# Kernel optimization log

Measured on AMD Instinct MI355X. Metric: run time of the kernel, lower is better.

## Reference

```python
import jax, jax.numpy as jnp
import numpy as np

NUM_HEADS = 16
NUM_KV_HEADS = 4
HEAD_DIM = 64
HIDDEN = 1024
B, S = 2, 2048


def setup_inputs() -> dict:
    key = jax.random.key(0)
    ks = jax.random.split(key, 9)
    sc = 0.02
    return {
        "x": jax.random.normal(ks[0], (B, S, HIDDEN), dtype=jnp.float32),
        "Wq": jax.random.normal(ks[1], (HIDDEN, NUM_HEADS * HEAD_DIM), dtype=jnp.float32) * sc,
        "bq": jnp.zeros((NUM_HEADS * HEAD_DIM,), dtype=jnp.float32),
        "Wk": jax.random.normal(ks[2], (HIDDEN, NUM_KV_HEADS * HEAD_DIM), dtype=jnp.float32) * sc,
        "bk": jnp.zeros((NUM_KV_HEADS * HEAD_DIM,), dtype=jnp.float32),
        "Wv": jax.random.normal(ks[3], (HIDDEN, NUM_KV_HEADS * HEAD_DIM), dtype=jnp.float32) * sc,
        "bv": jnp.zeros((NUM_KV_HEADS * HEAD_DIM,), dtype=jnp.float32),
        "Wo": jax.random.normal(ks[4], (NUM_HEADS * HEAD_DIM, HIDDEN), dtype=jnp.float32) * sc,
        "bo": jnp.zeros((HIDDEN,), dtype=jnp.float32),
    }


def reference(x, Wq, bq, Wk, bk, Wv, bv, Wo, bo):
    bs, seq, _ = x.shape
    groups = NUM_HEADS // NUM_KV_HEADS
    # projections -> [B, H, S, D]
    q = (x @ Wq + bq).reshape(bs, seq, NUM_HEADS, HEAD_DIM).transpose(0, 2, 1, 3)
    k = (x @ Wk + bk).reshape(bs, seq, NUM_KV_HEADS, HEAD_DIM).transpose(0, 2, 1, 3)
    v = (x @ Wv + bv).reshape(bs, seq, NUM_KV_HEADS, HEAD_DIM).transpose(0, 2, 1, 3)
    # repeat_interleave KV heads to match query heads (GQA expansion)
    k = jnp.repeat(k, groups, axis=1)
    v = jnp.repeat(v, groups, axis=1)
    # NOTE: source applies NO 1/sqrt(d) scaling and no mask/ALiBi
    scores = jnp.einsum("bhqd,bhkd->bhqk", q, k)
    attn = jax.nn.softmax(scores.astype(jnp.float32), axis=-1).astype(q.dtype)
    out = jnp.einsum("bhqk,bhkd->bhqd", attn, v)
    out = out.transpose(0, 2, 1, 3).reshape(bs, seq, NUM_HEADS * HEAD_DIM)
    return out @ Wo + bo
```

## Files before the change

### kernel.cpp

```cpp
#include <hip/hip_runtime.h>

#define NHEADS 16
#define NKV    4
#define HDIM   64
#define HIDDEN 1024
#define BATCH  2
#define SEQ    2048
#define MROWS  (BATCH * SEQ)
#define LOG2E  1.44269504088896340736f

typedef __bf16 bf16_t;
typedef bf16_t bf16x8 __attribute__((ext_vector_type(8)));
typedef float  f32x4  __attribute__((ext_vector_type(4)));

__device__ __forceinline__ float bf2f(unsigned short u) {
    return __uint_as_float(((unsigned int)u) << 16);
}
__device__ __forceinline__ unsigned short f2bf(float f) {
    unsigned int u = __float_as_uint(f);
    u += 0x7FFFu + ((u >> 16) & 1u);
    return (unsigned short)(u >> 16);
}

__device__ __forceinline__ void gld16(const unsigned short* g, unsigned short* l)
{
    __builtin_amdgcn_global_load_lds(
        (const __attribute__((address_space(1))) void*)g,
        (__attribute__((address_space(3))) void*)l,
        16, 0, 0);
}

__device__ __forceinline__ int swz(int row, int ch) {
    return (row * 8 + (ch ^ (row & 7))) * 8;
}
__device__ __forceinline__ int swz16(int row, int ch) {
    return (row * 16 + (ch ^ (row & 7))) * 8;
}

__device__ __forceinline__ bool sniff_is_f32(const unsigned short* __restrict__ x)
{
    const int e = (x[threadIdx.x & 63] >> 7) & 0xFF;
    const unsigned long long ok = __ballot(e >= 110 && e <= 140);
    return __popcll(ok) < 56;
}

__device__ __forceinline__ void load8cvt(const void* base, size_t elem, bool isf32, unsigned short out[8])
{
    if (!isf32) {
        *(uint4*)out = *(const uint4*)((const unsigned short*)base + elem);
    } else {
        const float* p = (const float*)base + elem;
        float4 v0 = *(const float4*)p;
        float4 v1 = *(const float4*)(p + 4);
        out[0] = f2bf(v0.x); out[1] = f2bf(v0.y); out[2] = f2bf(v0.z); out[3] = f2bf(v0.w);
        out[4] = f2bf(v1.x); out[5] = f2bf(v1.y); out[6] = f2bf(v1.z); out[7] = f2bf(v1.w);
    }
}
__device__ __forceinline__ float bias_at(const void* b, int i, bool isf32)
{
    return isf32 ? ((const float*)b)[i] : bf2f(((const unsigned short*)b)[i]);
}

__global__ __launch_bounds__(256)
void prep_kernel(const void* __restrict__ x,
                 const void* __restrict__ Wq, const void* __restrict__ Wk,
                 const void* __restrict__ Wv, const void* __restrict__ Wo,
                 unsigned short* __restrict__ xb,
                 unsigned short* __restrict__ Wqkvt,
                 unsigned short* __restrict__ Wot)
{
    const bool isf32 = sniff_is_f32((const unsigned short*)x);
    const int t = threadIdx.x;
    int bid = blockIdx.x;

    if (bid < 2048) {
        if (!isf32) return;
        const size_t c = (size_t)bid * 256 + t;
        unsigned short v[8];
        load8cvt(x, c * 8, true, v);
        *(uint4*)(&xb[c * 8]) = *(uint4*)v;
        return;
    }
    bid -= 2048;
    const void* src; unsigned short* dst; int N, rowoff;
    if (bid < 256)      {             src = Wq; dst = Wqkvt; N = 1024; rowoff = 0;    }
    else if (bid < 320) { bid -= 256; src = Wk; dst = Wqkvt; N = 256;  rowoff = 1024; }
    else if (bid < 384) { bid -= 320; src = Wv; dst = Wqkvt; N = 256;  rowoff = 1280; }
    else                { bid -= 384; src = Wo; dst = Wot;   N = 1024; rowoff = 0;    }
    const int ntx = N / 64;
    const int gn0 = (bid % ntx) * 64;
    const int gk0 = (bid / ntx) * 64;

    __shared__ unsigned short Ts[64][72];
#pragma unroll
    for (int half = 0; half < 2; ++half) {
        const int kl = (t >> 3) + half * 32;
        const int n8 = (t & 7) * 8;
        unsigned short v[8];
        load8cvt(src, (size_t)(gk0 + kl) * N + gn0 + n8, isf32, v);
        *(uint4*)(&Ts[kl][n8]) = *(uint4*)v;
    }
    __syncthreads();
#pragma unroll
    for (int half = 0; half < 2; ++half) {
        const int nl = (t >> 3) + half * 32;
        const int k8 = (t & 7) * 8;
        unsigned short v[8];
#pragma unroll
        for (int j = 0; j < 8; ++j) v[j] = Ts[k8 + j][nl];
        *(uint4*)(&dst[(size_t)(rowoff + gn0 + nl) * HIDDEN + gk0 + k8]) = *(uint4*)v;
    }
}

template<int TBM, int TBN>
__device__ __forceinline__ void gemm_tile(const unsigned short* __restrict__ A,
                                          const unsigned short* __restrict__ Bt,
                                          int K, int m0, int n0,
                                          unsigned short* As, unsigned short* Bs,
                                          f32x4 (&acc)[TBM / 32][TBN / 32])
{
    const int tid  = threadIdx.x;
    const int lane = tid & 63;
    const int wave = tid >> 6;
    const int quad = lane >> 4;
    const int l15  = lane & 15;
    const int wr   = wave >> 1;
    const int wc   = wave & 1;

    for (int k0 = 0; k0 < K; k0 += 128) {
#pragma unroll
        for (int r = 0; r < TBM / 16; ++r) {
            const int u = r * 256 + tid;
            const int row = u >> 4;
            const int gch = ((u & 15) ^ (row & 7)) * 8;
            gld16(&A[(size_t)(m0 + row) * K + k0 + gch], &As[(r * 256 + wave * 64) * 8]);
        }
#pragma unroll
        for (int r = 0; r < TBN / 16; ++r) {
            const int u = r * 256 + tid;
            const int row = u >> 4;
            const int gch = ((u & 15) ^ (row & 7)) * 8;
            gld16(&Bt[(size_t)(n0 + row) * K + k0 + gch], &Bs[(r * 256 + wave * 64) * 8]);
        }
        __syncthreads();

#pragma unroll
        for (int kk = 0; kk < 4; ++kk) {
            bf16x8 af[TBM / 32], bfv[TBN / 32];
#pragma unroll
            for (int i = 0; i < TBM / 32; ++i)
                af[i] = *(const bf16x8*)(&As[swz16(wr * (TBM / 2) + i * 16 + l15, kk * 4 + quad)]);
#pragma unroll
            for (int j = 0; j < TBN / 32; ++j)
                bfv[j] = *(const bf16x8*)(&Bs[swz16(wc * (TBN / 2) + j * 16 + l15, kk * 4 + quad)]);
#pragma unroll
            for (int i = 0; i < TBM / 32; ++i)
#pragma unroll
                for (int j = 0; j < TBN / 32; ++j)
                    acc[i][j] = __builtin_amdgcn_mfma_f32_16x16x32_bf16(af[i], bfv[j], acc[i][j], 0, 0, 0);
        }
        __syncthreads();
    }
}

__global__ __launch_bounds__(256)
void gemm_qkv(const void* __restrict__ xraw,
              const unsigned short* __restrict__ xb,
              const unsigned short* __restrict__ Bt,
              const void* __restrict__ bq, const void* __restrict__ bk,
              const void* __restrict__ bv,
              unsigned short* __restrict__ Qh,
              unsigned short* __restrict__ Kh,
              unsigned short* __restrict__ Vt)
{
    __shared__ __align__(16) unsigned short As[64 * 128];
    __shared__ __align__(16) unsigned short Bs[64 * 128];
    const bool bias_f32 = sniff_is_f32((const unsigned short*)xraw);
    const unsigned short* A = bias_f32 ? xb : (const unsigned short*)xraw;
    const int lane = threadIdx.x & 63;
    const int wave = threadIdx.x >> 6;
    const int quad = lane >> 4, l15 = lane & 15;
    const int wr = wave >> 1, wc = wave & 1;
    const int m0 = blockIdx.y * 64, n0 = blockIdx.x * 64;

    f32x4 acc[2][2] = {};
    gemm_tile<64, 64>(A, Bt, HIDDEN, m0, n0, As, Bs, acc);

#pragma unroll
    for (int i = 0; i < 2; ++i) {
#pragma unroll
        for (int j = 0; j < 2; ++j) {
            const int nn  = n0 + wc * 32 + j * 16 + l15;
            const int mmb = m0 + wr * 32 + i * 16 + quad * 4;
            const int b = mmb >> 11, s0 = mmb & 2047;
            if (nn < 1024) {
                const float bias = bias_at(bq, nn, bias_f32);
                const int h = nn >> 6, d = nn & 63;
                const size_t idx0 = (((size_t)(b * NHEADS + h)) * SEQ + s0) * 64 + d;
#pragma unroll
                for (int r = 0; r < 4; ++r)
                    Qh[idx0 + (size_t)r * 64] = f2bf((acc[i][j][r] + bias) * LOG2E);
            } else if (nn < 1280) {
                const int nk = nn - 1024;
                const float bias = bias_at(bk, nk, bias_f32);
                const int h = nk >> 6, d = nk & 63;
                const size_t idx0 = (((size_t)(b * NKV + h)) * SEQ + s0) * 64 + d;
#pragma unroll
                for (int r = 0; r < 4; ++r)
                    Kh[idx0 + (size_t)r * 64] = f2bf(acc[i][j][r] + bias);
            } else {
                const int nv = nn - 1280;
                const float bias = bias_at(bv, nv, bias_f32);
                const int h = nv >> 6, d = nv & 63;
                const size_t idx = (((size_t)(b * NKV + h)) * 64 + d) * SEQ + s0;
                unsigned short vv[4];
#pragma unroll
                for (int r = 0; r < 4; ++r) vv[r] = f2bf(acc[i][j][r] + bias);
                *(uint2*)(&Vt[idx]) = *(uint2*)vv;
            }
        }
    }
}

__global__ __launch_bounds__(256)
void gemm_o(const void* __restrict__ xraw,
            const unsigned short* __restrict__ A,
            const unsigned short* __restrict__ Bt,
            const void* __restrict__ bo,
            float* __restrict__ out)
{
    __shared__ __align__(16) unsigned short As[64 * 128];
    __shared__ __align__(16) unsigned short Bs[64 * 128];
    const bool bias_f32 = sniff_is_f32((const unsigned short*)xraw);
    const int lane = threadIdx.x & 63;
    const int wave = threadIdx.x >> 6;
    const int quad = lane >> 4, l15 = lane & 15;
    const int wr = wave >> 1, wc = wave & 1;
    const int m0 = blockIdx.y * 64, n0 = blockIdx.x * 64;

    f32x4 acc[2][2] = {};
    gemm_tile<64, 64>(A, Bt, HIDDEN, m0, n0, As, Bs, acc);

#pragma unroll
    for (int i = 0; i < 2; ++i) {
#pragma unroll
        for (int j = 0; j < 2; ++j) {
            const int nn = n0 + wc * 32 + j * 16 + l15;
            const float bvv = bias_at(bo, nn, bias_f32);
#pragma unroll
            for (int r = 0; r < 4; ++r) {
                const int mm = m0 + wr * 32 + i * 16 + quad * 4 + r;
                out[(size_t)mm * HIDDEN + nn] = acc[i][j][r] + bvv;
            }
        }
    }
}

#define PLD 68
__global__ __launch_bounds__(256)
void attn_kernel(const unsigned short* __restrict__ Qh,
                 const unsigned short* __restrict__ Kh,
                 const unsigned short* __restrict__ Vt,
                 unsigned short* __restrict__ O)
{
    __shared__ __align__(16) unsigned short Kth[64 * 64];
    __shared__ __align__(16) unsigned short VtT[64 * 64];
    __shared__ __align__(16) unsigned short Pt[4][16 * PLD];

    const int tid  = threadIdx.x;
    const int lane = tid & 63;
    const int wave = tid >> 6;
    const int quad = lane >> 4;
    const int l15  = lane & 15;

    const int qt = blockIdx.x;
    const int h  = blockIdx.y;
    const int b  = blockIdx.z;
    const int kv = h >> 2;

    const size_t qoff = ((size_t)(b * NHEADS + h)) * SEQ * HDIM;
    const size_t koff = ((size_t)(b * NKV + kv)) * SEQ * HDIM;
    const size_t voff = ((size_t)(b * NKV + kv)) * HDIM * SEQ;

    const int q0 = qt * 64 + wave * 16;

    const size_t qrow = qoff + (size_t)(q0 + l15) * HDIM;
    const bf16x8 qh0 = *(const bf16x8*)(&Qh[qrow + quad * 8]);
    const bf16x8 qh1 = *(const bf16x8*)(&Qh[qrow + 32 + quad * 8]);

    f32x4 o[4] = {};
    float lsum = 0.0f;

    const int srow0 = tid >> 3;
    const int schp  = tid & 7;

    const unsigned short* Khs = Kh + koff;
    const unsigned short* Vts = Vt + voff;

    for (int kt = 0; kt < SEQ / 64; ++kt, Khs += 64 * HDIM, Vts += 64) {
#pragma unroll
        for (int c = 0; c < 2; ++c) {
            const int row = srow0 + c * 32;
            const int gch = (schp ^ (row & 7)) * 8;
            gld16(&Khs[(size_t)row * 64 + gch],  &Kth[(c * 256 + wave * 64) * 8]);
            gld16(&Vts[(size_t)row * SEQ + gch], &VtT[(c * 256 + wave * 64) * 8]);
        }
        __syncthreads();

        f32x4 s[4];
#pragma unroll
        for (int j = 0; j < 4; ++j) {
            const int rr = j * 16 + l15;
            bf16x8 kh0 = *(const bf16x8*)(&Kth[swz(rr, quad)]);
            bf16x8 kh1 = *(const bf16x8*)(&Kth[swz(rr, quad ^ 4)]);
            f32x4 z = {};
            z = __builtin_amdgcn_mfma_f32_16x16x32_bf16(kh0, qh0, z, 0, 0, 0);
            s[j] = __builtin_amdgcn_mfma_f32_16x16x32_bf16(kh1, qh1, z, 0, 0, 0);
        }

#pragma unroll
        for (int j = 0; j < 4; ++j) {
            const float p0 = __builtin_amdgcn_exp2f(s[j][0]);
            const float p1 = __builtin_amdgcn_exp2f(s[j][1]);
            const float p2 = __builtin_amdgcn_exp2f(s[j][2]);
            const float p3 = __builtin_amdgcn_exp2f(s[j][3]);
            lsum += (p0 + p1) + (p2 + p3);
            uint2 w;
            w.x = __builtin_amdgcn_perm(__float_as_uint(p1), __float_as_uint(p0), 0x07060302u);
            w.y = __builtin_amdgcn_perm(__float_as_uint(p3), __float_as_uint(p2), 0x07060302u);
            *(uint2*)(&Pt[wave][l15 * PLD + j * 16 + quad * 4]) = w;
        }

#pragma unroll
        for (int kk = 0; kk < 2; ++kk) {
            bf16x8 pf = *(const bf16x8*)(&Pt[wave][l15 * PLD + kk * 32 + quad * 8]);
#pragma unroll
            for (int dt = 0; dt < 4; ++dt) {
                bf16x8 vf = *(const bf16x8*)(&VtT[swz(dt * 16 + l15, kk * 4 + quad)]);
                o[dt] = __builtin_amdgcn_mfma_f32_16x16x32_bf16(vf, pf, o[dt], 0, 0, 0);
            }
        }
        __syncthreads();
    }

    lsum += __shfl_xor(lsum, 16);
    lsum += __shfl_xor(lsum, 32);

    const float inv = 1.0f / lsum;
    const size_t rowbase = ((size_t)b * SEQ + (q0 + l15)) * (NHEADS * HDIM) + h * HDIM;
#pragma unroll
    for (int dt = 0; dt < 4; ++dt) {
        unsigned short v4[4];
#pragma unroll
        for (int r = 0; r < 4; ++r) v4[r] = f2bf(o[dt][r] * inv);
        *(uint2*)(&O[rowbase + dt * 16 + quad * 4]) = *(uint2*)v4;
    }
}

extern "C" void kernel_launch(void* const* d_in, const int* in_sizes, int n_in,
                              void* d_out, int out_size, void* d_ws, size_t ws_size,
                              hipStream_t stream)
{
    const void* x  = d_in[0];
    const void* Wq = d_in[1];
    const void* bq = d_in[2];
    const void* Wk = d_in[3];
    const void* bk = d_in[4];
    const void* Wv = d_in[5];
    const void* bv = d_in[6];
    const void* Wo = d_in[7];
    const void* bo = d_in[8];
    float* out = (float*)d_out;

    unsigned short* p = (unsigned short*)d_ws;
    unsigned short* xb    = p; p += (size_t)MROWS * HIDDEN;
    unsigned short* Wqkvt = p; p += (size_t)1536 * HIDDEN;
    unsigned short* Wot   = p; p += (size_t)HIDDEN * HIDDEN;
    unsigned short* Qh = p;  p += (size_t)MROWS * 1024;
    unsigned short* Kh = p;  p += (size_t)2 * NKV * SEQ * HDIM;
    unsigned short* Vt = p;  p += (size_t)2 * NKV * SEQ * HDIM;
    unsigned short* A2 = p;  p += (size_t)MROWS * 1024;

    dim3 blk(256);
    prep_kernel<<<dim3(2688), blk, 0, stream>>>(x, Wq, Wk, Wv, Wo, xb, Wqkvt, Wot);
    gemm_qkv<<<dim3(1536 / 64, MROWS / 64), blk, 0, stream>>>(
        x, xb, Wqkvt, bq, bk, bv, Qh, Kh, Vt);
    attn_kernel<<<dim3(SEQ / 64, NHEADS, BATCH), blk, 0, stream>>>(Qh, Kh, Vt, A2);
    gemm_o<<<dim3(1024 / 64, MROWS / 64), blk, 0, stream>>>(x, A2, Wot, bo, out);
}
```

Baseline: 186.5 us.

## Double-buffer attention K/V tiles, double query rows per wave, enlarge GEMM M tiles

The attention kernel now stages K/V tiles into two LDS buffers, prefetching the next tile while computing the current one, so there is one barrier per iteration instead of two. Each wave processes 32 query rows instead of 16, so each K/V fragment read is reused across two query sub-tiles and the attention grid halves. Both GEMMs move to 128x64 output tiles, giving more reuse of each B tile. The cost is more registers and LDS per block and fewer blocks in every kernel, which may lower occupancy.

```diff
diff --git a/kernel.cpp b/kernel.cpp
--- a/kernel.cpp
+++ b/kernel.cpp
@@ -173,7 +173,7 @@
               unsigned short* __restrict__ Kh,
               unsigned short* __restrict__ Vt)
 {
-    __shared__ __align__(16) unsigned short As[64 * 128];
+    __shared__ __align__(16) unsigned short As[128 * 128];
     __shared__ __align__(16) unsigned short Bs[64 * 128];
     const bool bias_f32 = sniff_is_f32((const unsigned short*)xraw);
     const unsigned short* A = bias_f32 ? xb : (const unsigned short*)xraw;
@@ -181,17 +181,17 @@
     const int wave = threadIdx.x >> 6;
     const int quad = lane >> 4, l15 = lane & 15;
     const int wr = wave >> 1, wc = wave & 1;
-    const int m0 = blockIdx.y * 64, n0 = blockIdx.x * 64;
-
-    f32x4 acc[2][2] = {};
-    gemm_tile<64, 64>(A, Bt, HIDDEN, m0, n0, As, Bs, acc);
-
-#pragma unroll
-    for (int i = 0; i < 2; ++i) {
+    const int m0 = blockIdx.y * 128, n0 = blockIdx.x * 64;
+
+    f32x4 acc[4][2] = {};
+    gemm_tile<128, 64>(A, Bt, HIDDEN, m0, n0, As, Bs, acc);
+
+#pragma unroll
+    for (int i = 0; i < 4; ++i) {
 #pragma unroll
         for (int j = 0; j < 2; ++j) {
             const int nn  = n0 + wc * 32 + j * 16 + l15;
-            const int mmb = m0 + wr * 32 + i * 16 + quad * 4;
+            const int mmb = m0 + wr * 64 + i * 16 + quad * 4;
             const int b = mmb >> 11, s0 = mmb & 2047;
             if (nn < 1024) {
                 const float bias = bias_at(bq, nn, bias_f32);
@@ -229,27 +229,27 @@
             const void* __restrict__ bo,
             float* __restrict__ out)
 {
-    __shared__ __align__(16) unsigned short As[64 * 128];
+    __shared__ __align__(16) unsigned short As[128 * 128];
     __shared__ __align__(16) unsigned short Bs[64 * 128];
     const bool bias_f32 = sniff_is_f32((const unsigned short*)xraw);
     const int lane = threadIdx.x & 63;
     const int wave = threadIdx.x >> 6;
     const int quad = lane >> 4, l15 = lane & 15;
     const int wr = wave >> 1, wc = wave & 1;
-    const int m0 = blockIdx.y * 64, n0 = blockIdx.x * 64;
-
-    f32x4 acc[2][2] = {};
-    gemm_tile<64, 64>(A, Bt, HIDDEN, m0, n0, As, Bs, acc);
-
-#pragma unroll
-    for (int i = 0; i < 2; ++i) {
+    const int m0 = blockIdx.y * 128, n0 = blockIdx.x * 64;
+
+    f32x4 acc[4][2] = {};
+    gemm_tile<128, 64>(A, Bt, HIDDEN, m0, n0, As, Bs, acc);
+
+#pragma unroll
+    for (int i = 0; i < 4; ++i) {
 #pragma unroll
         for (int j = 0; j < 2; ++j) {
             const int nn = n0 + wc * 32 + j * 16 + l15;
             const float bvv = bias_at(bo, nn, bias_f32);
 #pragma unroll
             for (int r = 0; r < 4; ++r) {
-                const int mm = m0 + wr * 32 + i * 16 + quad * 4 + r;
+                const int mm = m0 + wr * 64 + i * 16 + quad * 4 + r;
                 out[(size_t)mm * HIDDEN + nn] = acc[i][j][r] + bvv;
             }
         }
@@ -257,15 +257,34 @@
 }
 
 #define PLD 68
+#define NT  (SEQ / 64)
+
+__device__ __forceinline__ void attn_stage(const unsigned short* __restrict__ Kt,
+                                           const unsigned short* __restrict__ Vtc,
+                                           unsigned short* Kd, unsigned short* Vd,
+                                           int tid)
+{
+    const int wave  = tid >> 6;
+    const int srow0 = tid >> 3;
+    const int schp  = tid & 7;
+#pragma unroll
+    for (int c = 0; c < 2; ++c) {
+        const int row = srow0 + c * 32;
+        const int gch = (schp ^ (row & 7)) * 8;
+        gld16(&Kt[(size_t)row * HDIM + gch], &Kd[(c * 256 + wave * 64) * 8]);
+        gld16(&Vtc[(size_t)row * SEQ + gch], &Vd[(c * 256 + wave * 64) * 8]);
+    }
+}
+
 __global__ __launch_bounds__(256)
 void attn_kernel(const unsigned short* __restrict__ Qh,
                  const unsigned short* __restrict__ Kh,
                  const unsigned short* __restrict__ Vt,
                  unsigned short* __restrict__ O)
 {
-    __shared__ __align__(16) unsigned short Kth[64 * 64];
-    __shared__ __align__(16) unsigned short VtT[64 * 64];
-    __shared__ __align__(16) unsigned short Pt[4][16 * PLD];
+    __shared__ __align__(16) unsigned short Kth[2][64 * 64];
+    __shared__ __align__(16) unsigned short VtT[2][64 * 64];
+    __shared__ __align__(16) unsigned short Pt[4][32 * PLD];
 
     const int tid  = threadIdx.x;
     const int lane = tid & 63;
@@ -282,78 +301,87 @@
     const size_t koff = ((size_t)(b * NKV + kv)) * SEQ * HDIM;
     const size_t voff = ((size_t)(b * NKV + kv)) * HDIM * SEQ;
 
-    const int q0 = qt * 64 + wave * 16;
-
-    const size_t qrow = qoff + (size_t)(q0 + l15) * HDIM;
-    const bf16x8 qh0 = *(const bf16x8*)(&Qh[qrow + quad * 8]);
-    const bf16x8 qh1 = *(const bf16x8*)(&Qh[qrow + 32 + quad * 8]);
-
-    f32x4 o[4] = {};
-    float lsum = 0.0f;
-
-    const int srow0 = tid >> 3;
-    const int schp  = tid & 7;
+    const int q0 = qt * 128 + wave * 32;
+
+    bf16x8 qf0[2], qf1[2];
+#pragma unroll
+    for (int qs = 0; qs < 2; ++qs) {
+        const size_t qrow = qoff + (size_t)(q0 + qs * 16 + l15) * HDIM;
+        qf0[qs] = *(const bf16x8*)(&Qh[qrow + quad * 8]);
+        qf1[qs] = *(const bf16x8*)(&Qh[qrow + 32 + quad * 8]);
+    }
+
+    f32x4 o0[4] = {}, o1[4] = {};
+    f32x4 ls0 = {}, ls1 = {};
 
     const unsigned short* Khs = Kh + koff;
     const unsigned short* Vts = Vt + voff;
 
-    for (int kt = 0; kt < SEQ / 64; ++kt, Khs += 64 * HDIM, Vts += 64) {
-#pragma unroll
-        for (int c = 0; c < 2; ++c) {
-            const int row = srow0 + c * 32;
-            const int gch = (schp ^ (row & 7)) * 8;
-            gld16(&Khs[(size_t)row * 64 + gch],  &Kth[(c * 256 + wave * 64) * 8]);
-            gld16(&Vts[(size_t)row * SEQ + gch], &VtT[(c * 256 + wave * 64) * 8]);
-        }
+    attn_stage(Khs, Vts, &Kth[0][0], &VtT[0][0], tid);
+
+    for (int kt = 0; kt < NT; ++kt) {
         __syncthreads();
-
-        f32x4 s[4];
+        const int cur = kt & 1;
+        if (kt + 1 < NT)
+            attn_stage(Khs + (size_t)(kt + 1) * 64 * HDIM,
+                       Vts + (size_t)(kt + 1) * 64,
+                       &Kth[cur ^ 1][0], &VtT[cur ^ 1][0], tid);
+
+        const unsigned short* Kc = &Kth[cur][0];
+        const unsigned short* Vc = &VtT[cur][0];
+
 #pragma unroll
         for (int j = 0; j < 4; ++j) {
             const int rr = j * 16 + l15;
-            bf16x8 kh0 = *(const bf16x8*)(&Kth[swz(rr, quad)]);
-            bf16x8 kh1 = *(const bf16x8*)(&Kth[swz(rr, quad ^ 4)]);
-            f32x4 z = {};
-            z = __builtin_amdgcn_mfma_f32_16x16x32_bf16(kh0, qh0, z, 0, 0, 0);
-            s[j] = __builtin_amdgcn_mfma_f32_16x16x32_bf16(kh1, qh1, z, 0, 0, 0);
-        }
-
-#pragma unroll
-        for (int j = 0; j < 4; ++j) {
-            const float p0 = __builtin_amdgcn_exp2f(s[j][0]);
-            const float p1 = __builtin_amdgcn_exp2f(s[j][1]);
-            const float p2 = __builtin_amdgcn_exp2f(s[j][2]);
-            const float p3 = __builtin_amdgcn_exp2f(s[j][3]);
-            lsum += (p0 + p1) + (p2 + p3);
-            uint2 w;
-            w.x = __builtin_amdgcn_perm(__float_as_uint(p1), __float_as_uint(p0), 0x07060302u);
-            w.y = __builtin_amdgcn_perm(__float_as_uint(p3), __float_as_uint(p2), 0x07060302u);
-            *(uint2*)(&Pt[wave][l15 * PLD + j * 16 + quad * 4]) = w;
+            const bf16x8 kh0 = *(const bf16x8*)(&Kc[swz(rr, quad)]);
+            const bf16x8 kh1 = *(const bf16x8*)(&Kc[swz(rr, quad ^ 4)]);
+#pragma unroll
+            for (int qs = 0; qs < 2; ++qs) {
+                f32x4 z = {};
+                z = __builtin_amdgcn_mfma_f32_16x16x32_bf16(kh0, qs ? qf0[1] : qf0[0], z, 0, 0, 0);
+                const f32x4 sc = __builtin_amdgcn_mfma_f32_16x16x32_bf16(kh1, qs ? qf1[1] : qf1[0], z, 0, 0, 0);
+                const float p0 = __builtin_amdgcn_exp2f(sc[0]);
+                const float p1 = __builtin_amdgcn_exp2f(sc[1]);
+                const float p2 = __builtin_amdgcn_exp2f(sc[2]);
+                const float p3 = __builtin_amdgcn_exp2f(sc[3]);
+                const f32x4 pv = {p0, p1, p2, p3};
+                if (qs == 0) ls0 += pv; else ls1 += pv;
+                uint2 w;
+                w.x = __builtin_amdgcn_perm(__float_as_uint(p1), __float_as_uint(p0), 0x07060302u);
+                w.y = __builtin_amdgcn_perm(__float_as_uint(p3), __float_as_uint(p2), 0x07060302u);
+                *(uint2*)(&Pt[wave][(qs * 16 + l15) * PLD + j * 16 + quad * 4]) = w;
+            }
         }
 
 #pragma unroll
         for (int kk = 0; kk < 2; ++kk) {
-            bf16x8 pf = *(const bf16x8*)(&Pt[wave][l15 * PLD + kk * 32 + quad * 8]);
+            const bf16x8 pf0 = *(const bf16x8*)(&Pt[wave][l15 * PLD + kk * 32 + quad * 8]);
+            const bf16x8 pf1 = *(const bf16x8*)(&Pt[wave][(16 + l15) * PLD + kk * 32 + quad * 8]);
 #pragma unroll
             for (int dt = 0; dt < 4; ++dt) {
-                bf16x8 vf = *(const bf16x8*)(&VtT[swz(dt * 16 + l15, kk * 4 + quad)]);
-                o[dt] = __builtin_amdgcn_mfma_f32_16x16x32_bf16(vf, pf, o[dt], 0, 0, 0);
+                const bf16x8 vf = *(const bf16x8*)(&Vc[swz(dt * 16 + l15, kk * 4 + quad)]);
+                o0[dt] = __builtin_amdgcn_mfma_f32_16x16x32_bf16(vf, pf0, o0[dt], 0, 0, 0);
+                o1[dt] = __builtin_amdgcn_mfma_f32_16x16x32_bf16(vf, pf1, o1[dt], 0, 0, 0);
             }
         }
-        __syncthreads();
-    }
-
-    lsum += __shfl_xor(lsum, 16);
-    lsum += __shfl_xor(lsum, 32);
-
-    const float inv = 1.0f / lsum;
-    const size_t rowbase = ((size_t)b * SEQ + (q0 + l15)) * (NHEADS * HDIM) + h * HDIM;
-#pragma unroll
-    for (int dt = 0; dt < 4; ++dt) {
-        unsigned short v4[4];
-#pragma unroll
-        for (int r = 0; r < 4; ++r) v4[r] = f2bf(o[dt][r] * inv);
-        *(uint2*)(&O[rowbase + dt * 16 + quad * 4]) = *(uint2*)v4;
+    }
+
+#pragma unroll
+    for (int qs = 0; qs < 2; ++qs) {
+        const f32x4 lv = qs ? ls1 : ls0;
+        float lsum = (lv[0] + lv[1]) + (lv[2] + lv[3]);
+        lsum += __shfl_xor(lsum, 16);
+        lsum += __shfl_xor(lsum, 32);
+        const float inv = 1.0f / lsum;
+        const size_t rowbase = ((size_t)b * SEQ + (q0 + qs * 16 + l15)) * (NHEADS * HDIM) + h * HDIM;
+#pragma unroll
+        for (int dt = 0; dt < 4; ++dt) {
+            const f32x4 ov = qs ? o1[dt] : o0[dt];
+            unsigned short v4[4];
+#pragma unroll
+            for (int r = 0; r < 4; ++r) v4[r] = f2bf(ov[r] * inv);
+            *(uint2*)(&O[rowbase + dt * 16 + quad * 4]) = *(uint2*)v4;
+        }
     }
 }
 
@@ -383,8 +411,8 @@
 
     dim3 blk(256);
     prep_kernel<<<dim3(2688), blk, 0, stream>>>(x, Wq, Wk, Wv, Wo, xb, Wqkvt, Wot);
-    gemm_qkv<<<dim3(1536 / 64, MROWS / 64), blk, 0, stream>>>(
+    gemm_qkv<<<dim3(1536 / 64, MROWS / 128), blk, 0, stream>>>(
         x, xb, Wqkvt, bq, bk, bv, Qh, Kh, Vt);
-    attn_kernel<<<dim3(SEQ / 64, NHEADS, BATCH), blk, 0, stream>>>(Qh, Kh, Vt, A2);
-    gemm_o<<<dim3(1024 / 64, MROWS / 64), blk, 0, stream>>>(x, A2, Wot, bo, out);
-}
+    attn_kernel<<<dim3(SEQ / 128, NHEADS, BATCH), blk, 0, stream>>>(Qh, Kh, Vt, A2);
+    gemm_o<<<dim3(1024 / 64, MROWS / 128), blk, 0, stream>>>(x, A2, Wot, bo, out);
+}
```

Measured after the change: 185.6 us. About the same (-0.5%).
